# Kernel tuning notes

Measured on AMD Instinct MI355X. Metric: run time of the kernel, lower is better.

Reference implementation:

```python
import jax, jax.numpy as jnp
import numpy as np

PERI_IDX = np.array([0, 1, 2, 3, 5, 6, 7, 8])  # non-center taps of the 3x3 window


def _extract_patches(x, stride, padding):
    # x: [B,C,H,W] -> patches [B,C,9,Hout,Wout], tap k = di*3+dj (row-major), matching F.unfold.
    B, C, H, W = x.shape
    Hout = (H + 2 * padding - 3) // stride + 1
    Wout = (W + 2 * padding - 3) // stride + 1
    xp = jnp.pad(x, ((0, 0), (0, 0), (padding, padding), (padding, padding)))
    taps = [xp[:, :, di:di + (Hout - 1) * stride + 1:stride, dj:dj + (Wout - 1) * stride + 1:stride]
            for di in range(3) for dj in range(3)]
    return jnp.stack(taps, axis=2)  # [B,C,9,Hout,Wout]


def setup_inputs() -> dict:
    key = jax.random.key(0)
    k1, k2, k3, k4 = jax.random.split(key, 4)
    B, C, O, H, W = 8, 64, 64, 128, 128
    x = jax.random.normal(k1, (B, C, H, W), dtype=jnp.float32)
    core = jax.random.normal(k2, (O, C, 1, 1), dtype=jnp.float32) * (1.0 / np.sqrt(C))
    periphery = jax.random.uniform(k3, (8,), dtype=jnp.float32, minval=-0.1, maxval=0.1)
    threshold = jnp.array([0.1], dtype=jnp.float32)
    scale = jnp.array([10.0], dtype=jnp.float32)
    return {"x": x, "core": core, "periphery": periphery, "threshold": threshold,
            "scale": scale, "stride": 1, "padding": 1}


def reference(x, core, periphery, threshold, scale, stride, padding):
    B, C, H, W = x.shape
    O = core.shape[0]
    patches = _extract_patches(x, stride, padding)           # [B,C,9,Ho,Wo]
    center = patches[:, :, 4]                                 # [B,C,Ho,Wo]
    # per-pixel variance-like routing statistic over channels and taps
    div = jnp.sum((patches - center[:, :, None]) ** 2, axis=(1, 2))  # [B,Ho,Wo]
    m_hard = jax.nn.sigmoid((div - threshold[0]) * scale[0]) > 0.5   # [B,Ho,Wo] bool
    w = core.reshape(O, C)
    # path 0 (low variance): 1x1 conv on the center pixel
    zero_out = jnp.einsum('bchw,oc->bohw', center, w)
    # path 1 (high variance): periphery-weighted sum then 1x1 conv
    agg = jnp.einsum('bckhw,k->bchw', patches[:, :, PERI_IDX], periphery)
    one_out = jnp.einsum('bchw,oc->bohw', agg, w)
    return jnp.where(m_hard[:, None], one_out, zero_out)
```

## Files before the change

kernel.cpp:

```cpp
#include <hip/hip_runtime.h>
#include <hip/hip_bf16.h>

constexpr int Bc = 8;
constexpr int Cc = 64;
constexpr int Oc = 64;
constexpr int Hc = 128;
constexpr int Wc = 128;
constexpr int HWc = Hc * Wc;
constexpr int CP = 72;

typedef __attribute__((ext_vector_type(8))) short short8;
typedef __attribute__((ext_vector_type(4))) float floatx4;
typedef __attribute__((ext_vector_type(2))) float floatx2;

__device__ __forceinline__ float bperm(int idx4, float v) {
    return __int_as_float(__builtin_amdgcn_ds_bpermute(idx4, __float_as_int(v)));
}
__device__ __forceinline__ unsigned cvt_pk_bf16(float lo, float hi) {
    unsigned r;
    asm("v_cvt_pk_bf16_f32 %0, %1, %2" : "=v"(r) : "v"(lo), "v"(hi));
    return r;
}

__global__ __launch_bounds__(256, 4) void spconv_kernel(
    const float* __restrict__ x, const float* __restrict__ core,
    const float* __restrict__ peri, const float* __restrict__ thr,
    const float* __restrict__ scl, float* __restrict__ out)
{
    __shared__ __hip_bfloat16 s_selT[Wc][CP];
    __shared__ float s_divp[4][Wc];
    __shared__ float s_msk[Wc];

    const int tid = threadIdx.x;
    const int l   = tid & 63;
    const int wv  = tid >> 6;
    const int b   = blockIdx.x & 7;
    const int h   = blockIdx.x >> 3;

    const int o0   = wv * 16;
    const int n    = l & 15;
    const int quad = l >> 4;

    const float* arow = core + (size_t)(o0 + n) * Cc + quad * 8;
    const floatx4 af0 = *(const floatx4*)(arow);
    const floatx4 af1 = *(const floatx4*)(arow + 4);
    const floatx4 af2 = *(const floatx4*)(arow + 32);
    const floatx4 af3 = *(const floatx4*)(arow + 36);
    union { unsigned u[4]; short8 s; } A0, A1;
    A0.u[0] = cvt_pk_bf16(af0.x, af0.y); A0.u[1] = cvt_pk_bf16(af0.z, af0.w);
    A0.u[2] = cvt_pk_bf16(af1.x, af1.y); A0.u[3] = cvt_pk_bf16(af1.z, af1.w);
    A1.u[0] = cvt_pk_bf16(af2.x, af2.y); A1.u[1] = cvt_pk_bf16(af2.z, af2.w);
    A1.u[2] = cvt_pk_bf16(af3.x, af3.y); A1.u[3] = cvt_pk_bf16(af3.z, af3.w);

    const int upIdx = ((l - 1) & 63) << 2;
    const int dnIdx = ((l + 1) & 63) << 2;
    const float lzf = (l == 0)  ? 0.f : 1.f;
    const float rzf = (l == 63) ? 0.f : 1.f;
    const float mUf = (h > 0) ? 1.f : 0.f;
    const float mDf = (h < Hc - 1) ? 1.f : 0.f;
    const int   dU  = (h > 0) ? -Wc : 0;
    const int   dD  = (h < Hc - 1) ? Wc : 0;

    const float p0 = peri[0], p1 = peri[1], p2 = peri[2], p3 = peri[3];
    const float p4 = peri[4], p5 = peri[5], p6 = peri[6], p7 = peri[7];
    const float thrv = thr[0], sclv = scl[0];

    const float* xw = x + (size_t)b * Cc * HWc + (size_t)h * Wc + 2 * l;
    const float* xb = x + (size_t)b * Cc * HWc + (size_t)h * Wc;

    float dlo = 0.f, dhi = 0.f;

#define PROC1(RM, R0, R1, K) do {                                             \
    const float rmL = lzf * bperm(upIdx, RM.y);                               \
    const float r0L = lzf * bperm(upIdx, R0.y);                               \
    const float r1L = lzf * bperm(upIdx, R1.y);                               \
    const float rmR = rzf * bperm(dnIdx, RM.x);                               \
    const float r0R = rzf * bperm(dnIdx, R0.x);                               \
    const float r1R = rzf * bperm(dnIdx, R1.x);                               \
    { const float t = R0.x;                              \
      float a = p0 * rmL; a = fmaf(p1, RM.x, a); a = fmaf(p2, RM.y, a);       \
      a = fmaf(p3, r0L, a); a = fmaf(p4, R0.y, a);                            \
      a = fmaf(p5, r1L, a); a = fmaf(p6, R1.x, a); a = fmaf(p7, R1.y, a);     \
      aLo[K] = a; float e;                                                    \
      e = rmL  - t; dlo = fmaf(e, e, dlo); e = RM.x - t; dlo = fmaf(e, e, dlo); \
      e = RM.y - t; dlo = fmaf(e, e, dlo); e = r0L  - t; dlo = fmaf(e, e, dlo); \
      e = R0.y - t; dlo = fmaf(e, e, dlo); e = r1L  - t; dlo = fmaf(e, e, dlo); \
      e = R1.x - t; dlo = fmaf(e, e, dlo); e = R1.y - t; dlo = fmaf(e, e, dlo); } \
    { const float t = R0.y;                            \
      float a = p0 * RM.x; a = fmaf(p1, RM.y, a); a = fmaf(p2, rmR, a);       \
      a = fmaf(p3, R0.x, a); a = fmaf(p4, r0R, a);                            \
      a = fmaf(p5, R1.x, a); a = fmaf(p6, R1.y, a); a = fmaf(p7, r1R, a);     \
      aHi[K] = a; float e;                                                    \
      e = RM.x - t; dhi = fmaf(e, e, dhi); e = RM.y - t; dhi = fmaf(e, e, dhi); \
      e = rmR  - t; dhi = fmaf(e, e, dhi); e = R0.x - t; dhi = fmaf(e, e, dhi); \
      e = r0R  - t; dhi = fmaf(e, e, dhi); e = R1.x - t; dhi = fmaf(e, e, dhi); \
      e = R1.y - t; dhi = fmaf(e, e, dhi); e = r1R  - t; dhi = fmaf(e, e, dhi); } \
} while (0)

    #pragma unroll 2
    for (int j = 0; j < 8; ++j) {
        const int c0 = wv * 16 + 2 * j;
        const float* b0p = xw + (size_t)c0 * HWc;
        const float* b1p = b0p + HWc;

        floatx2 rm0 = *(const floatx2*)(b0p + dU);
        floatx2 r00 = *(const floatx2*)(b0p);
        floatx2 r10 = *(const floatx2*)(b0p + dD);
        floatx2 rm1 = *(const floatx2*)(b1p + dU);
        floatx2 r01 = *(const floatx2*)(b1p);
        floatx2 r11 = *(const floatx2*)(b1p + dD);
        rm0 *= mUf; r10 *= mDf; rm1 *= mUf; r11 *= mDf;

        float aLo[2], aHi[2];
        PROC1(rm0, r00, r10, 0);
        PROC1(rm1, r01, r11, 1);

        *(unsigned*)&s_selT[l]      [c0] = cvt_pk_bf16(aLo[0], aLo[1]);
        *(unsigned*)&s_selT[64 + l] [c0] = cvt_pk_bf16(aHi[0], aHi[1]);
    }
#undef PROC1

    {
        floatx2 dv = {dlo, dhi};
        *(floatx2*)&s_divp[wv][2 * l] = dv;
    }
    __syncthreads();

    floatx2 sum2 = {0.f, 0.f};
    #pragma unroll
    for (int g = 0; g < 4; ++g)
        sum2 += *(const floatx2*)&s_divp[g][2 * l];
    const bool badLo = ((sum2.x - thrv) * sclv) <= 0.f;
    const bool badHi = ((sum2.y - thrv) * sclv) <= 0.f;
    if (__any(badLo || badHi)) {
        if (wv == 0) {
            s_msk[2 * l]     = badLo ? 0.f : 1.f;
            s_msk[2 * l + 1] = badHi ? 0.f : 1.f;
        }
        __syncthreads();
        #pragma unroll
        for (int i = 0; i < 32; ++i) {
            const int idx = i * 256 + tid;
            const int p   = idx & (Wc - 1);
            const int c   = idx >> 7;
            const int ww  = ((p & 63) << 1) | (p >> 6);
            if (s_msk[ww] == 0.f)
                s_selT[p][c] = __float2bfloat16(xb[(size_t)c * HWc + ww]);
        }
        __syncthreads();
    }

    float* outb = out + ((size_t)(b * Oc) * Hc + h) * Wc;

    __builtin_amdgcn_s_setprio(1);
    #pragma unroll
    for (int t = 0; t < 8; ++t) {
        const int w0   = t * 16;
        const int wlog = w0 + n;
        const int pr   = ((wlog >> 1) & 63) | ((wlog & 1) << 6);
        const short8 b0 = *(const short8*)&s_selT[pr][quad * 8];
        const short8 b1 = *(const short8*)&s_selT[pr][quad * 8 + 32];
        floatx4 acc = {0.f, 0.f, 0.f, 0.f};
        acc = __builtin_amdgcn_mfma_f32_16x16x32_bf16(A0.s, b0, acc, 0, 0, 0);
        acc = __builtin_amdgcn_mfma_f32_16x16x32_bf16(A1.s, b1, acc, 0, 0, 0);
        #pragma unroll
        for (int r = 0; r < 4; ++r) {
            const int o = o0 + quad * 4 + r;
            outb[(size_t)o * HWc + w0 + n] = acc[r];
        }
    }
    __builtin_amdgcn_s_setprio(0);
}

extern "C" void kernel_launch(void* const* d_in, const int* in_sizes, int n_in,
                              void* d_out, int out_size, void* d_ws, size_t ws_size,
                              hipStream_t stream) {
    const float* x    = (const float*)d_in[0];
    const float* core = (const float*)d_in[1];
    const float* peri = (const float*)d_in[2];
    const float* thr  = (const float*)d_in[3];
    const float* scl  = (const float*)d_in[4];
    float* out = (float*)d_out;

    spconv_kernel<<<dim3(Bc * Hc), dim3(256), 0, stream>>>(
        x, core, peri, thr, scl, out);
}
```

Measured before the change: 99.78 us.

## Process four rows per block with rolling row registers and double-buffered LDS

Each block now handles four consecutive output rows with 512 threads. Input rows are kept in a rolling U/M/D register window, so each input row is loaded about once per block instead of three times. The next row is prefetched while the current one is processed, and the LDS buffers are double-buffered. Channels are split across 8 waves and width tiles across the two halves of the block for the MFMA stage. The grid shrinks to 256 blocks, which may underfill the GPU's CUs, and register pressure rises from holding 24 float2 rows plus prefetches.

```diff
diff --git a/kernel.cpp b/kernel.cpp
--- a/kernel.cpp
+++ b/kernel.cpp
@@ -22,22 +22,24 @@
     return r;
 }
 
-__global__ __launch_bounds__(256, 4) void spconv_kernel(
+__global__ __launch_bounds__(512, 2) void spconv_kernel(
     const float* __restrict__ x, const float* __restrict__ core,
     const float* __restrict__ peri, const float* __restrict__ thr,
     const float* __restrict__ scl, float* __restrict__ out)
 {
-    __shared__ __hip_bfloat16 s_selT[Wc][CP];
-    __shared__ float s_divp[4][Wc];
+    __shared__ __hip_bfloat16 s_selT[2][Wc][CP];
+    __shared__ float s_divp[2][8][Wc];
     __shared__ float s_msk[Wc];
 
-    const int tid = threadIdx.x;
-    const int l   = tid & 63;
-    const int wv  = tid >> 6;
-    const int b   = blockIdx.x & 7;
-    const int h   = blockIdx.x >> 3;
-
-    const int o0   = wv * 16;
+    const int tid  = threadIdx.x;
+    const int l    = tid & 63;
+    const int wv   = tid >> 6;
+    const int b    = blockIdx.x & 7;
+    const int rblk = blockIdx.x >> 3;
+    const int h0   = rblk * 4;
+
+    const int o0   = (wv & 3) * 16;
+    const int wh   = wv >> 2;
     const int n    = l & 15;
     const int quad = l >> 4;
 
@@ -56,19 +58,23 @@
     const int dnIdx = ((l + 1) & 63) << 2;
     const float lzf = (l == 0)  ? 0.f : 1.f;
     const float rzf = (l == 63) ? 0.f : 1.f;
-    const float mUf = (h > 0) ? 1.f : 0.f;
-    const float mDf = (h < Hc - 1) ? 1.f : 0.f;
-    const int   dU  = (h > 0) ? -Wc : 0;
-    const int   dD  = (h < Hc - 1) ? Wc : 0;
 
     const float p0 = peri[0], p1 = peri[1], p2 = peri[2], p3 = peri[3];
     const float p4 = peri[4], p5 = peri[5], p6 = peri[6], p7 = peri[7];
     const float thrv = thr[0], sclv = scl[0];
 
-    const float* xw = x + (size_t)b * Cc * HWc + (size_t)h * Wc + 2 * l;
-    const float* xb = x + (size_t)b * Cc * HWc + (size_t)h * Wc;
-
-    float dlo = 0.f, dhi = 0.f;
+    const int   c0 = wv * 8;
+    const float* xl = x + (size_t)b * Cc * HWc + 2 * l;
+    const int hUm = (h0 > 0) ? h0 - 1 : 0;
+
+    floatx2 U[8], M[8], D[8];
+    #pragma unroll
+    for (int j = 0; j < 8; ++j) {
+        const float* pc = xl + (size_t)(c0 + j) * HWc;
+        U[j] = *(const floatx2*)(pc + hUm * Wc);
+        M[j] = *(const floatx2*)(pc + h0 * Wc);
+        D[j] = *(const floatx2*)(pc + (h0 + 1) * Wc);
+    }
 
 #define PROC1(RM, R0, R1, K) do {                                             \
     const float rmL = lzf * bperm(upIdx, RM.y);                               \
@@ -97,79 +103,95 @@
       e = R1.y - t; dhi = fmaf(e, e, dhi); e = r1R  - t; dhi = fmaf(e, e, dhi); } \
 } while (0)
 
-    #pragma unroll 2
-    for (int j = 0; j < 8; ++j) {
-        const int c0 = wv * 16 + 2 * j;
-        const float* b0p = xw + (size_t)c0 * HWc;
-        const float* b1p = b0p + HWc;
-
-        floatx2 rm0 = *(const floatx2*)(b0p + dU);
-        floatx2 r00 = *(const floatx2*)(b0p);
-        floatx2 r10 = *(const floatx2*)(b0p + dD);
-        floatx2 rm1 = *(const floatx2*)(b1p + dU);
-        floatx2 r01 = *(const floatx2*)(b1p);
-        floatx2 r11 = *(const floatx2*)(b1p + dD);
-        rm0 *= mUf; r10 *= mDf; rm1 *= mUf; r11 *= mDf;
-
-        float aLo[2], aHi[2];
-        PROC1(rm0, r00, r10, 0);
-        PROC1(rm1, r01, r11, 1);
-
-        *(unsigned*)&s_selT[l]      [c0] = cvt_pk_bf16(aLo[0], aLo[1]);
-        *(unsigned*)&s_selT[64 + l] [c0] = cvt_pk_bf16(aHi[0], aHi[1]);
+    #pragma unroll
+    for (int it = 0; it < 4; ++it) {
+        const int h   = h0 + it;
+        const int buf = it & 1;
+
+        floatx2 N[8];
+        if (it < 3) {
+            const int hN = (h + 2 < Hc) ? h + 2 : Hc - 1;
+            #pragma unroll
+            for (int j = 0; j < 8; ++j)
+                N[j] = *(const floatx2*)(xl + (size_t)(c0 + j) * HWc + hN * Wc);
+        }
+
+        const float mUf = (h > 0) ? 1.f : 0.f;
+        const float mDf = (h < Hc - 1) ? 1.f : 0.f;
+
+        float dlo = 0.f, dhi = 0.f;
+        #pragma unroll
+        for (int jp = 0; jp < 4; ++jp) {
+            const int cA = c0 + 2 * jp;
+            floatx2 rm0 = U[2 * jp]     * mUf;
+            floatx2 r00 = M[2 * jp];
+            floatx2 r10 = D[2 * jp]     * mDf;
+            floatx2 rm1 = U[2 * jp + 1] * mUf;
+            floatx2 r01 = M[2 * jp + 1];
+            floatx2 r11 = D[2 * jp + 1] * mDf;
+
+            float aLo[2], aHi[2];
+            PROC1(rm0, r00, r10, 0);
+            PROC1(rm1, r01, r11, 1);
+
+            *(unsigned*)&s_selT[buf][l]      [cA] = cvt_pk_bf16(aLo[0], aLo[1]);
+            *(unsigned*)&s_selT[buf][64 + l] [cA] = cvt_pk_bf16(aHi[0], aHi[1]);
+        }
+        {   floatx2 dv = {dlo, dhi};
+            *(floatx2*)&s_divp[buf][wv][2 * l] = dv;
+        }
+        __syncthreads();
+
+        floatx2 sum2 = {0.f, 0.f};
+        #pragma unroll
+        for (int g = 0; g < 8; ++g)
+            sum2 += *(const floatx2*)&s_divp[buf][g][2 * l];
+        const bool badLo = ((sum2.x - thrv) * sclv) <= 0.f;
+        const bool badHi = ((sum2.y - thrv) * sclv) <= 0.f;
+        if (__any(badLo || badHi)) {
+            if (wv == 0) {
+                s_msk[2 * l]     = badLo ? 0.f : 1.f;
+                s_msk[2 * l + 1] = badHi ? 0.f : 1.f;
+            }
+            __syncthreads();
+            const float* xbh = x + (size_t)b * Cc * HWc + (size_t)h * Wc;
+            #pragma unroll
+            for (int i = 0; i < 16; ++i) {
+                const int idx = i * 512 + tid;
+                const int p   = idx & (Wc - 1);
+                const int c   = idx >> 7;
+                const int ww  = ((p & 63) << 1) | (p >> 6);
+                if (s_msk[ww] == 0.f)
+                    s_selT[buf][p][c] =
+                        __float2bfloat16(xbh[(size_t)c * HWc + ww]);
+            }
+            __syncthreads();
+        }
+
+        float* outb = out + ((size_t)(b * Oc) * Hc + h) * Wc;
+        #pragma unroll
+        for (int t = 0; t < 4; ++t) {
+            const int w0   = (wh * 4 + t) * 16;
+            const int wlog = w0 + n;
+            const int pr   = ((wlog >> 1) & 63) | ((wlog & 1) << 6);
+            const short8 b0f = *(const short8*)&s_selT[buf][pr][quad * 8];
+            const short8 b1f = *(const short8*)&s_selT[buf][pr][quad * 8 + 32];
+            floatx4 acc = {0.f, 0.f, 0.f, 0.f};
+            acc = __builtin_amdgcn_mfma_f32_16x16x32_bf16(A0.s, b0f, acc, 0, 0, 0);
+            acc = __builtin_amdgcn_mfma_f32_16x16x32_bf16(A1.s, b1f, acc, 0, 0, 0);
+            #pragma unroll
+            for (int r = 0; r < 4; ++r) {
+                const int o = o0 + quad * 4 + r;
+                outb[(size_t)o * HWc + w0 + n] = acc[r];
+            }
+        }
+
+        if (it < 3) {
+            #pragma unroll
+            for (int j = 0; j < 8; ++j) { U[j] = M[j]; M[j] = D[j]; D[j] = N[j]; }
+        }
     }
 #undef PROC1
-
-    {
-        floatx2 dv = {dlo, dhi};
-        *(floatx2*)&s_divp[wv][2 * l] = dv;
-    }
-    __syncthreads();
-
-    floatx2 sum2 = {0.f, 0.f};
-    #pragma unroll
-    for (int g = 0; g < 4; ++g)
-        sum2 += *(const floatx2*)&s_divp[g][2 * l];
-    const bool badLo = ((sum2.x - thrv) * sclv) <= 0.f;
-    const bool badHi = ((sum2.y - thrv) * sclv) <= 0.f;
-    if (__any(badLo || badHi)) {
-        if (wv == 0) {
-            s_msk[2 * l]     = badLo ? 0.f : 1.f;
-            s_msk[2 * l + 1] = badHi ? 0.f : 1.f;
-        }
-        __syncthreads();
-        #pragma unroll
-        for (int i = 0; i < 32; ++i) {
-            const int idx = i * 256 + tid;
-            const int p   = idx & (Wc - 1);
-            const int c   = idx >> 7;
-            const int ww  = ((p & 63) << 1) | (p >> 6);
-            if (s_msk[ww] == 0.f)
-                s_selT[p][c] = __float2bfloat16(xb[(size_t)c * HWc + ww]);
-        }
-        __syncthreads();
-    }
-
-    float* outb = out + ((size_t)(b * Oc) * Hc + h) * Wc;
-
-    __builtin_amdgcn_s_setprio(1);
-    #pragma unroll
-    for (int t = 0; t < 8; ++t) {
-        const int w0   = t * 16;
-        const int wlog = w0 + n;
-        const int pr   = ((wlog >> 1) & 63) | ((wlog & 1) << 6);
-        const short8 b0 = *(const short8*)&s_selT[pr][quad * 8];
-        const short8 b1 = *(const short8*)&s_selT[pr][quad * 8 + 32];
-        floatx4 acc = {0.f, 0.f, 0.f, 0.f};
-        acc = __builtin_amdgcn_mfma_f32_16x16x32_bf16(A0.s, b0, acc, 0, 0, 0);
-        acc = __builtin_amdgcn_mfma_f32_16x16x32_bf16(A1.s, b1, acc, 0, 0, 0);
-        #pragma unroll
-        for (int r = 0; r < 4; ++r) {
-            const int o = o0 + quad * 4 + r;
-            outb[(size_t)o * HWc + w0 + n] = acc[r];
-        }
-    }
-    __builtin_amdgcn_s_setprio(0);
 }
 
 extern "C" void kernel_launch(void* const* d_in, const int* in_sizes, int n_in,
@@ -182,6 +204,6 @@
     const float* scl  = (const float*)d_in[4];
     float* out = (float*)d_out;
 
-    spconv_kernel<<<dim3(Bc * Hc), dim3(256), 0, stream>>>(
+    spconv_kernel<<<dim3(Bc * Hc / 4), dim3(512), 0, stream>>>(
         x, core, peri, thr, scl, out);
 }
```

New measurement: 100.2 us. About the same (+0.4%).

## Split fused kernel into selection kernel and GEMM kernel via workspace

Applied to the files above, without the earlier changes.

Splits the single fused kernel into two launches. The first computes the routing statistic and the selected bf16 input (aggregated or center) per pixel and writes it to a global workspace in pixel-major layout. The second loads that workspace and runs the 1x1 conv with MFMA. This removes the LDS transpose buffer and the conditional global reload of center pixels for low-variance pixels. In exchange it adds a second launch and a round trip of about 16 MB of bf16 through global memory, though that may stay in cache.

```diff
diff --git a/kernel.cpp b/kernel.cpp
--- a/kernel.cpp
+++ b/kernel.cpp
@@ -7,11 +7,11 @@
 constexpr int Hc = 128;
 constexpr int Wc = 128;
 constexpr int HWc = Hc * Wc;
-constexpr int CP = 72;
 
 typedef __attribute__((ext_vector_type(8))) short short8;
 typedef __attribute__((ext_vector_type(4))) float floatx4;
 typedef __attribute__((ext_vector_type(2))) float floatx2;
+typedef __attribute__((ext_vector_type(4))) unsigned uintx4;
 
 __device__ __forceinline__ float bperm(int idx4, float v) {
     return __int_as_float(__builtin_amdgcn_ds_bpermute(idx4, __float_as_int(v)));
@@ -22,35 +22,19 @@
     return r;
 }
 
-__global__ __launch_bounds__(256, 4) void spconv_kernel(
-    const float* __restrict__ x, const float* __restrict__ core,
-    const float* __restrict__ peri, const float* __restrict__ thr,
-    const float* __restrict__ scl, float* __restrict__ out)
+__global__ __launch_bounds__(256, 4) void sel_kernel(
+    const float* __restrict__ x, const float* __restrict__ peri,
+    const float* __restrict__ thr, const float* __restrict__ scl,
+    unsigned short* __restrict__ selws)
 {
-    __shared__ __hip_bfloat16 s_selT[Wc][CP];
     __shared__ float s_divp[4][Wc];
-    __shared__ float s_msk[Wc];
 
     const int tid = threadIdx.x;
     const int l   = tid & 63;
     const int wv  = tid >> 6;
     const int b   = blockIdx.x & 7;
     const int h   = blockIdx.x >> 3;
-
-    const int o0   = wv * 16;
-    const int n    = l & 15;
-    const int quad = l >> 4;
-
-    const float* arow = core + (size_t)(o0 + n) * Cc + quad * 8;
-    const floatx4 af0 = *(const floatx4*)(arow);
-    const floatx4 af1 = *(const floatx4*)(arow + 4);
-    const floatx4 af2 = *(const floatx4*)(arow + 32);
-    const floatx4 af3 = *(const floatx4*)(arow + 36);
-    union { unsigned u[4]; short8 s; } A0, A1;
-    A0.u[0] = cvt_pk_bf16(af0.x, af0.y); A0.u[1] = cvt_pk_bf16(af0.z, af0.w);
-    A0.u[2] = cvt_pk_bf16(af1.x, af1.y); A0.u[3] = cvt_pk_bf16(af1.z, af1.w);
-    A1.u[0] = cvt_pk_bf16(af2.x, af2.y); A1.u[1] = cvt_pk_bf16(af2.z, af2.w);
-    A1.u[2] = cvt_pk_bf16(af3.x, af3.y); A1.u[3] = cvt_pk_bf16(af3.z, af3.w);
+    const int c0  = wv * 16;
 
     const int upIdx = ((l - 1) & 63) << 2;
     const int dnIdx = ((l + 1) & 63) << 2;
@@ -66,9 +50,9 @@
     const float thrv = thr[0], sclv = scl[0];
 
     const float* xw = x + (size_t)b * Cc * HWc + (size_t)h * Wc + 2 * l;
-    const float* xb = x + (size_t)b * Cc * HWc + (size_t)h * Wc;
 
     float dlo = 0.f, dhi = 0.f;
+    unsigned aggLoPk[8], aggHiPk[8], cenLoPk[8], cenHiPk[8];
 
 #define PROC1(RM, R0, R1, K) do {                                             \
     const float rmL = lzf * bperm(upIdx, RM.y);                               \
@@ -99,8 +83,8 @@
 
     #pragma unroll 2
     for (int j = 0; j < 8; ++j) {
-        const int c0 = wv * 16 + 2 * j;
-        const float* b0p = xw + (size_t)c0 * HWc;
+        const int cA = c0 + 2 * j;
+        const float* b0p = xw + (size_t)cA * HWc;
         const float* b1p = b0p + HWc;
 
         floatx2 rm0 = *(const floatx2*)(b0p + dU);
@@ -115,13 +99,14 @@
         PROC1(rm0, r00, r10, 0);
         PROC1(rm1, r01, r11, 1);
 
-        *(unsigned*)&s_selT[l]      [c0] = cvt_pk_bf16(aLo[0], aLo[1]);
-        *(unsigned*)&s_selT[64 + l] [c0] = cvt_pk_bf16(aHi[0], aHi[1]);
+        aggLoPk[j] = cvt_pk_bf16(aLo[0], aLo[1]);
+        aggHiPk[j] = cvt_pk_bf16(aHi[0], aHi[1]);
+        cenLoPk[j] = cvt_pk_bf16(r00.x, r01.x);
+        cenHiPk[j] = cvt_pk_bf16(r00.y, r01.y);
     }
 #undef PROC1
 
-    {
-        floatx2 dv = {dlo, dhi};
+    {   floatx2 dv = {dlo, dhi};
         *(floatx2*)&s_divp[wv][2 * l] = dv;
     }
     __syncthreads();
@@ -130,46 +115,69 @@
     #pragma unroll
     for (int g = 0; g < 4; ++g)
         sum2 += *(const floatx2*)&s_divp[g][2 * l];
-    const bool badLo = ((sum2.x - thrv) * sclv) <= 0.f;
-    const bool badHi = ((sum2.y - thrv) * sclv) <= 0.f;
-    if (__any(badLo || badHi)) {
-        if (wv == 0) {
-            s_msk[2 * l]     = badLo ? 0.f : 1.f;
-            s_msk[2 * l + 1] = badHi ? 0.f : 1.f;
-        }
-        __syncthreads();
-        #pragma unroll
-        for (int i = 0; i < 32; ++i) {
-            const int idx = i * 256 + tid;
-            const int p   = idx & (Wc - 1);
-            const int c   = idx >> 7;
-            const int ww  = ((p & 63) << 1) | (p >> 6);
-            if (s_msk[ww] == 0.f)
-                s_selT[p][c] = __float2bfloat16(xb[(size_t)c * HWc + ww]);
-        }
-        __syncthreads();
+    const bool oneLo = ((sum2.x - thrv) * sclv) > 0.f;
+    const bool oneHi = ((sum2.y - thrv) * sclv) > 0.f;
+
+    uintx4 sLo0, sLo1, sHi0, sHi1;
+    #pragma unroll
+    for (int i = 0; i < 4; ++i) {
+        sLo0[i] = oneLo ? aggLoPk[i]     : cenLoPk[i];
+        sLo1[i] = oneLo ? aggLoPk[i + 4] : cenLoPk[i + 4];
+        sHi0[i] = oneHi ? aggHiPk[i]     : cenHiPk[i];
+        sHi1[i] = oneHi ? aggHiPk[i + 4] : cenHiPk[i + 4];
     }
 
-    float* outb = out + ((size_t)(b * Oc) * Hc + h) * Wc;
+    unsigned short* sb =
+        selws + ((size_t)(b * HWc + h * Wc + 2 * l)) * Cc + c0;
+    *(uintx4*)(sb)           = sLo0;
+    *(uintx4*)(sb + 8)       = sLo1;
+    *(uintx4*)(sb + Cc)      = sHi0;
+    *(uintx4*)(sb + Cc + 8)  = sHi1;
+}
 
-    __builtin_amdgcn_s_setprio(1);
+__global__ __launch_bounds__(256, 4) void gemm_kernel(
+    const float* __restrict__ core,
+    const unsigned short* __restrict__ selws, float* __restrict__ out)
+{
+    const int tid = threadIdx.x;
+    const int l   = tid & 63;
+    const int wv  = tid >> 6;
+    const int b   = blockIdx.x & 7;
+    const int pc  = blockIdx.x >> 3;
+    const int p0  = pc * 128;
+
+    const int o0   = wv * 16;
+    const int n    = l & 15;
+    const int quad = l >> 4;
+
+    const float* arow = core + (size_t)(o0 + n) * Cc + quad * 8;
+    const floatx4 af0 = *(const floatx4*)(arow);
+    const floatx4 af1 = *(const floatx4*)(arow + 4);
+    const floatx4 af2 = *(const floatx4*)(arow + 32);
+    const floatx4 af3 = *(const floatx4*)(arow + 36);
+    union { unsigned u[4]; short8 s; } A0, A1;
+    A0.u[0] = cvt_pk_bf16(af0.x, af0.y); A0.u[1] = cvt_pk_bf16(af0.z, af0.w);
+    A0.u[2] = cvt_pk_bf16(af1.x, af1.y); A0.u[3] = cvt_pk_bf16(af1.z, af1.w);
+    A1.u[0] = cvt_pk_bf16(af2.x, af2.y); A1.u[1] = cvt_pk_bf16(af2.z, af2.w);
+    A1.u[2] = cvt_pk_bf16(af3.x, af3.y); A1.u[3] = cvt_pk_bf16(af3.z, af3.w);
+
+    const unsigned short* sb = selws + (size_t)b * HWc * Cc;
+    float* outb = out + (size_t)b * Oc * HWc;
+
     #pragma unroll
     for (int t = 0; t < 8; ++t) {
-        const int w0   = t * 16;
-        const int wlog = w0 + n;
-        const int pr   = ((wlog >> 1) & 63) | ((wlog & 1) << 6);
-        const short8 b0 = *(const short8*)&s_selT[pr][quad * 8];
-        const short8 b1 = *(const short8*)&s_selT[pr][quad * 8 + 32];
+        const int p = p0 + t * 16 + n;
+        const short8 b0 = *(const short8*)(sb + (size_t)p * Cc + quad * 8);
+        const short8 b1 = *(const short8*)(sb + (size_t)p * Cc + 32 + quad * 8);
         floatx4 acc = {0.f, 0.f, 0.f, 0.f};
         acc = __builtin_amdgcn_mfma_f32_16x16x32_bf16(A0.s, b0, acc, 0, 0, 0);
         acc = __builtin_amdgcn_mfma_f32_16x16x32_bf16(A1.s, b1, acc, 0, 0, 0);
         #pragma unroll
         for (int r = 0; r < 4; ++r) {
             const int o = o0 + quad * 4 + r;
-            outb[(size_t)o * HWc + w0 + n] = acc[r];
+            outb[(size_t)o * HWc + p] = acc[r];
         }
     }
-    __builtin_amdgcn_s_setprio(0);
 }
 
 extern "C" void kernel_launch(void* const* d_in, const int* in_sizes, int n_in,
@@ -181,7 +189,10 @@
     const float* thr  = (const float*)d_in[3];
     const float* scl  = (const float*)d_in[4];
     float* out = (float*)d_out;
+    unsigned short* selws = (unsigned short*)d_ws;
 
-    spconv_kernel<<<dim3(Bc * Hc), dim3(256), 0, stream>>>(
-        x, core, peri, thr, scl, out);
+    sel_kernel<<<dim3(Bc * Hc), dim3(256), 0, stream>>>(
+        x, peri, thr, scl, selws);
+    gemm_kernel<<<dim3(Bc * Hc), dim3(256), 0, stream>>>(
+        core, selws, out);
 }
```

Result: slower. 127.8 us (+28.1%).
